# Kernel optimization log

Hardware: AMD Instinct MI355X
Metric: run time of the kernel (lower is better)

The kernel has to match this reference:

```python
import jax, jax.numpy as jnp
import numpy as np

N, E, D, H, G, C = 50000, 800000, 3, 128, 64, 10

def setup_inputs() -> dict:
    key = jax.random.key(0)
    ks = jax.random.split(key, 10)
    s = 0.1  # small init scale
    return {
        "pos": jax.random.normal(ks[0], (N, D), jnp.float32),
        "edge_index": jax.random.randint(ks[1], (2, E), 0, N, dtype=jnp.int64),
        "batch": jnp.sort(jax.random.randint(ks[2], (N,), 0, G, dtype=jnp.int64)),
        "W1": jax.random.normal(ks[3], (D, H), jnp.float32) * s,
        "b1": jnp.zeros((H,), jnp.float32),
        "W2": jax.random.normal(ks[4], (H, H), jnp.float32) * s,
        "b2": jnp.zeros((H,), jnp.float32),
        "W3": jax.random.normal(ks[5], (H, H), jnp.float32) * s,
        "b3": jnp.zeros((H,), jnp.float32),
        "Wl1": jax.random.normal(ks[6], (H, H // 2), jnp.float32) * s,
        "bl1": jnp.zeros((H // 2,), jnp.float32),
        "Wl2": jax.random.normal(ks[7], (H // 2, C), jnp.float32) * s,
        "bl2": jnp.zeros((C,), jnp.float32),
        "num_graphs": G,
    }

def reference(pos, edge_index, batch, W1, b1, W2, b2, W3, b3, Wl1, bl1, Wl2, bl2, num_graphs):
    n = pos.shape[0]
    loop = jnp.arange(n, dtype=edge_index.dtype)
    # GCN: add self-loops, symmetric normalization deg^-1/2 (A+I) deg^-1/2
    src = jnp.concatenate([edge_index[0], loop])
    dst = jnp.concatenate([edge_index[1], loop])
    deg = jax.ops.segment_sum(jnp.ones(src.shape, pos.dtype), dst, num_segments=n)
    dinv = jax.lax.rsqrt(jnp.maximum(deg, 1e-12))  # deg >= 1 due to self-loops
    norm = dinv[src] * dinv[dst]  # [E+N]

    def gcn(x, W, b):
        h = x @ W                               # [N,F] dense transform first (PyG order)
        msg = h[src] * norm[:, None]            # gather + normalize
        return jax.ops.segment_sum(msg, dst, num_segments=n) + b  # scatter-add

    x = jax.nn.relu(gcn(pos, W1, b1))   # dropout = identity (eval mode)
    x = jax.nn.relu(gcn(x, W2, b2))
    x = jax.nn.relu(gcn(x, W3, b3))
    # global_mean_pool over batch ids
    sums = jax.ops.segment_sum(x, batch, num_segments=num_graphs)
    cnt = jax.ops.segment_sum(jnp.ones((n,), x.dtype), batch, num_segments=num_graphs)
    g = sums / jnp.maximum(cnt, 1.0)[:, None]   # [G,H]
    h = jax.nn.relu(g @ Wl1 + bl1)
    return h @ Wl2 + bl2
```

## Files before the change

kernel.cpp:

```cpp
#include <hip/hip_runtime.h>

#define H 128
#define CAP 64
#define LSTRIDE 136
#define PSTR 132
typedef unsigned int uint32;
typedef unsigned short ushort16;
typedef __attribute__((ext_vector_type(8))) short bf16x8;
typedef __attribute__((ext_vector_type(4))) float f32x4;

static __device__ __forceinline__ ushort16 f2bf(float f){
  uint32 u = __float_as_uint(f);
  uint32 r = (u + 0x7fff + ((u >> 16) & 1)) >> 16;
  return (ushort16)r;
}
static __device__ __forceinline__ float bflo(uint32 u){ return __uint_as_float(u << 16); }
static __device__ __forceinline__ float bfhi(uint32 u){ return __uint_as_float(u & 0xffff0000u); }

__global__ __launch_bounds__(256) void k_setup(int* __restrict__ deg, float* __restrict__ gsum,
                                               const int* __restrict__ batch, int n, int G,
                                               int* __restrict__ gb, int SB,
                                               const float* __restrict__ W2, const float* __restrict__ W3,
                                               ushort16* __restrict__ wp2, ushort16* __restrict__ wp3,
                                               float4* __restrict__ y0,
                                               unsigned short* __restrict__ ybA,
                                               unsigned short* __restrict__ ybB,
                                               uint4* __restrict__ csr4){
  int b = blockIdx.x;
  if (b < SB){
    int i = b*256 + threadIdx.x;
    int T = SB*256;
    uint32 ss = (uint32)n | ((uint32)n << 16);
    int NB = (n+1)*8;
    for (int j = i; j < NB; j += T){
      uint4 v; v.x = ss; v.y = ss; v.z = ss; v.w = ss;
      if ((j & 7) == 0){
        int node = j >> 3;
        v.x = (uint32)((node < n)? node : n) | ((uint32)n << 16);
      }
      csr4[j] = v;
    }
    if (i < n) deg[i] = 1;
    if (i < G*H) gsum[i] = 0.f;
    if (i < H){ ybA[(size_t)n*H + i] = 0; ybB[(size_t)n*H + i] = 0; }
    if (i == 0) y0[n] = make_float4(0.f, 0.f, 0.f, 0.f);
    if (i <= G){
      int lo = 0, hi = n;
      while (lo < hi){ int m = (lo + hi) >> 1; if (batch[m] < i) lo = m + 1; else hi = m; }
      gb[i] = lo;
    }
  } else {
    int gid = (b - SB)*256 + threadIdx.x;
    const float* W = (gid < 2048) ? W2 : W3;
    ushort16* wp   = (gid < 2048) ? wp2 : wp3;
    int tid = gid & 2047;
    int frag = tid >> 6, lane = tid & 63;
    int kt = frag >> 3, ct = frag & 7;
    int m = lane & 15, quad = lane >> 4;
    const float* wrow = &W[(kt*32 + quad*8)*H + ct*16 + m];
    ushort16 vals[8];
    #pragma unroll
    for (int j = 0; j < 8; j++) vals[j] = f2bf(wrow[j*H]);
    uint4 o;
    o.x = (uint32)vals[0] | ((uint32)vals[1] << 16);
    o.y = (uint32)vals[2] | ((uint32)vals[3] << 16);
    o.z = (uint32)vals[4] | ((uint32)vals[5] << 16);
    o.w = (uint32)vals[6] | ((uint32)vals[7] << 16);
    *(uint4*)&wp[(size_t)tid*8] = o;
  }
}

__global__ __launch_bounds__(256) void k_fill(const int* __restrict__ src, const int* __restrict__ dst,
                                              int E, int* __restrict__ deg,
                                              unsigned short* __restrict__ csr_src){
  int i = blockIdx.x*256 + threadIdx.x;
  if (i < E){
    int d = dst[i];
    int slot = atomicAdd(&deg[d], 1);
    if (slot < CAP) csr_src[((size_t)d << 6) + slot] = (unsigned short)src[i];
  }
}

__global__ __launch_bounds__(256) void k_pre(const int* __restrict__ deg, const float* __restrict__ pos,
                                             float4* __restrict__ y0, int n){
  int i = blockIdx.x*256 + threadIdx.x;
  if (i < n){
    float dv = rsqrtf((float)deg[i]);
    y0[i] = make_float4(pos[3*i]*dv, pos[3*i+1]*dv, pos[3*i+2]*dv, 0.f);
  }
}

__global__ __launch_bounds__(256) void k_layer1(const float4* __restrict__ y0, const int* __restrict__ deg,
      const unsigned short* __restrict__ csr_src,
      const float* __restrict__ W1, const float* __restrict__ b1,
      ushort16* __restrict__ y1, int n){
  int node = blockIdx.x*256 + threadIdx.x;
  if (node >= n) return;
  int cnt = deg[node];
  int lo = node << 6;
  int hi = lo + ((cnt + 7) & ~7);
  float x=0.f, y=0.f, z=0.f;
  uint4 iv = *(const uint4*)&csr_src[lo];
  for (int e = lo; e < hi; e += 8){
    uint4 ivn = *(const uint4*)&csr_src[e + 8];
    int s0 = iv.x & 0xffff, s1 = iv.x >> 16;
    int s2 = iv.y & 0xffff, s3 = iv.y >> 16;
    int s4 = iv.z & 0xffff, s5 = iv.z >> 16;
    int s6 = iv.w & 0xffff, s7 = iv.w >> 16;
    float4 v0 = y0[s0], v1 = y0[s1], v2 = y0[s2], v3 = y0[s3];
    float4 v4 = y0[s4], v5 = y0[s5], v6 = y0[s6], v7 = y0[s7];
    x += ((v0.x+v1.x)+(v2.x+v3.x)) + ((v4.x+v5.x)+(v6.x+v7.x));
    y += ((v0.y+v1.y)+(v2.y+v3.y)) + ((v4.y+v5.y)+(v6.y+v7.y));
    z += ((v0.z+v1.z)+(v2.z+v3.z)) + ((v4.z+v5.z)+(v6.z+v7.z));
    iv = ivn;
  }
  float dn = rsqrtf((float)cnt);
  x *= dn; y *= dn; z *= dn;
  ushort16* rowp = &y1[(size_t)node*H];
  for (int c8 = 0; c8 < 16; c8++){
    float4 wa0 = *(const float4*)&W1[c8*8];
    float4 wa1 = *(const float4*)&W1[c8*8+4];
    float4 wb0 = *(const float4*)&W1[H + c8*8];
    float4 wb1 = *(const float4*)&W1[H + c8*8+4];
    float4 wc0 = *(const float4*)&W1[2*H + c8*8];
    float4 wc1 = *(const float4*)&W1[2*H + c8*8+4];
    float4 bb0 = *(const float4*)&b1[c8*8];
    float4 bb1 = *(const float4*)&b1[c8*8+4];
    float o0 = fmaxf(x*wa0.x + y*wb0.x + z*wc0.x + bb0.x, 0.f) * dn;
    float o1 = fmaxf(x*wa0.y + y*wb0.y + z*wc0.y + bb0.y, 0.f) * dn;
    float o2 = fmaxf(x*wa0.z + y*wb0.z + z*wc0.z + bb0.z, 0.f) * dn;
    float o3 = fmaxf(x*wa0.w + y*wb0.w + z*wc0.w + bb0.w, 0.f) * dn;
    float o4 = fmaxf(x*wa1.x + y*wb1.x + z*wc1.x + bb1.x, 0.f) * dn;
    float o5 = fmaxf(x*wa1.y + y*wb1.y + z*wc1.y + bb1.y, 0.f) * dn;
    float o6 = fmaxf(x*wa1.z + y*wb1.z + z*wc1.z + bb1.z, 0.f) * dn;
    float o7 = fmaxf(x*wa1.w + y*wb1.w + z*wc1.w + bb1.w, 0.f) * dn;
    uint4 o;
    o.x = (uint32)f2bf(o0) | ((uint32)f2bf(o1) << 16);
    o.y = (uint32)f2bf(o2) | ((uint32)f2bf(o3) << 16);
    o.z = (uint32)f2bf(o4) | ((uint32)f2bf(o5) << 16);
    o.w = (uint32)f2bf(o6) | ((uint32)f2bf(o7) << 16);
    *(uint4*)&rowp[c8*8] = o;
  }
}

template<int POOL>
__global__ __launch_bounds__(256) void k_aggdense(const ushort16* __restrict__ y, const int* __restrict__ deg,
      const unsigned short* __restrict__ csr_src, const ushort16* __restrict__ wp,
      const float* __restrict__ bias,
      ushort16* __restrict__ yout, const int* __restrict__ batch, float* __restrict__ gsum, int n){
  __shared__ unsigned short As[16*LSTRIDE];
  __shared__ float pool[POOL ? 16*PSTR : 1];
  __shared__ unsigned short outs[POOL ? 1 : 16*PSTR];
  __shared__ int sbatch[POOL ? 16 : 1];
  __shared__ float sdinv[POOL ? 1 : 16];
  int tid = threadIdx.x;
  int node16 = blockIdx.x*16;
  int nl = tid >> 4;
  int node = node16 + nl;
  int f8 = (tid & 15) * 8;

  if (tid < 16){
    int nn = node16 + tid;
    if (POOL) sbatch[tid] = (nn < n) ? batch[nn] : -1;
    else      sdinv[tid]  = (nn < n) ? rsqrtf((float)deg[nn]) : 0.f;
  }

  float a0=0,a1=0,a2=0,a3=0,a4=0,a5=0,a6=0,a7=0;
  float dn = 0.f;
  #define ADDU(u) { a0+=bflo(u.x); a1+=bfhi(u.x); a2+=bflo(u.y); a3+=bfhi(u.y); \
                    a4+=bflo(u.z); a5+=bfhi(u.z); a6+=bflo(u.w); a7+=bfhi(u.w); }
  if (node < n){
    int cnt = deg[node];
    int lo = node << 6;
    int hi = lo + ((cnt + 7) & ~7);
    dn = rsqrtf((float)cnt);
    uint4 iv = *(const uint4*)&csr_src[lo];
    for (int e = lo; e < hi; e += 8){
      uint4 ivn = *(const uint4*)&csr_src[e + 8];
      int s0 = iv.x & 0xffff, s1 = iv.x >> 16;
      int s2 = iv.y & 0xffff, s3 = iv.y >> 16;
      int s4 = iv.z & 0xffff, s5 = iv.z >> 16;
      int s6 = iv.w & 0xffff, s7 = iv.w >> 16;
      uint4 u0 = *(const uint4*)&y[(size_t)s0*H + f8];
      uint4 u1 = *(const uint4*)&y[(size_t)s1*H + f8];
      uint4 u2 = *(const uint4*)&y[(size_t)s2*H + f8];
      uint4 u3 = *(const uint4*)&y[(size_t)s3*H + f8];
      uint4 u4 = *(const uint4*)&y[(size_t)s4*H + f8];
      uint4 u5 = *(const uint4*)&y[(size_t)s5*H + f8];
      uint4 u6 = *(const uint4*)&y[(size_t)s6*H + f8];
      uint4 u7 = *(const uint4*)&y[(size_t)s7*H + f8];
      ADDU(u0); ADDU(u1); ADDU(u2); ADDU(u3);
      ADDU(u4); ADDU(u5); ADDU(u6); ADDU(u7);
      iv = ivn;
    }
  }
  #undef ADDU
  uint4 o;
  o.x = (uint32)f2bf(a0*dn) | ((uint32)f2bf(a1*dn) << 16);
  o.y = (uint32)f2bf(a2*dn) | ((uint32)f2bf(a3*dn) << 16);
  o.z = (uint32)f2bf(a4*dn) | ((uint32)f2bf(a5*dn) << 16);
  o.w = (uint32)f2bf(a6*dn) | ((uint32)f2bf(a7*dn) << 16);
  *(uint4*)&As[nl*LSTRIDE + f8] = o;
  __syncthreads();

  int wave = tid >> 6;
  int lane = tid & 63;
  int m = lane & 15, quad = lane >> 4;
  f32x4 acc0 = {0.f,0.f,0.f,0.f}, acc1 = {0.f,0.f,0.f,0.f};
  int ct0 = wave*2, ct1 = wave*2 + 1;
  #pragma unroll
  for (int kt = 0; kt < 4; kt++){
    bf16x8 af = *(const bf16x8*)&As[m*LSTRIDE + kt*32 + quad*8];
    bf16x8 b0 = *(const bf16x8*)&wp[(size_t)((kt*8+ct0)*64 + lane)*8];
    bf16x8 b1 = *(const bf16x8*)&wp[(size_t)((kt*8+ct1)*64 + lane)*8];
    acc0 = __builtin_amdgcn_mfma_f32_16x16x32_bf16(af, b0, acc0, 0, 0, 0);
    acc1 = __builtin_amdgcn_mfma_f32_16x16x32_bf16(af, b1, acc1, 0, 0, 0);
  }
  #pragma unroll
  for (int j = 0; j < 2; j++){
    int ct = wave*2 + j;
    int col = ct*16 + m;
    float bv = bias[col];
    f32x4 ac = j ? acc1 : acc0;
    #pragma unroll
    for (int r = 0; r < 4; r++){
      int rl = quad*4 + r;
      int orow = node16 + rl;
      if (orow < n){
        float v = fmaxf(ac[r] + bv, 0.f);
        if (POOL) pool[rl*PSTR + col] = v;
        else      outs[rl*PSTR + col] = f2bf(v * sdinv[rl]);
      }
    }
  }
  __syncthreads();
  if (POOL){
    int col = tid & 127;
    int half = tid >> 7;
    float run = 0.f; int gprev = -1;
    for (int r = half*8; r < half*8 + 8; r++){
      int g = sbatch[r];
      if (g < 0) break;
      if (g != gprev){
        if (gprev >= 0) atomicAdd(&gsum[gprev*H + col], run);
        run = 0.f; gprev = g;
      }
      run += pool[r*PSTR + col];
    }
    if (gprev >= 0) atomicAdd(&gsum[gprev*H + col], run);
  } else {
    int row = tid >> 4;
    int orow = node16 + row;
    if (orow < n){
      const unsigned short* sp = &outs[row*PSTR + f8];
      uint4 v;
      v.x = (uint32)sp[0] | ((uint32)sp[1] << 16);
      v.y = (uint32)sp[2] | ((uint32)sp[3] << 16);
      v.z = (uint32)sp[4] | ((uint32)sp[5] << 16);
      v.w = (uint32)sp[6] | ((uint32)sp[7] << 16);
      *(uint4*)&yout[(size_t)orow*H + f8] = v;
    }
  }
}

__global__ __launch_bounds__(64) void k_head(const float* __restrict__ gsum, const int* __restrict__ gb,
            const float* __restrict__ Wl1, const float* __restrict__ bl1,
            const float* __restrict__ Wl2, const float* __restrict__ bl2,
            float* __restrict__ out){
  int g = blockIdx.x;
  int t = threadIdx.x;
  __shared__ float gs[H];
  __shared__ float h1[64];
  float inv = 1.f / fmaxf((float)(gb[g+1] - gb[g]), 1.f);
  gs[t]      = gsum[g*H + t]      * inv;
  gs[64 + t] = gsum[g*H + 64 + t] * inv;
  __syncthreads();
  float acc = bl1[t];
  for (int k = 0; k < H; k++) acc += gs[k] * Wl1[k*64 + t];
  h1[t] = fmaxf(acc, 0.f);
  __syncthreads();
  if (t < 10){
    float o = bl2[t];
    for (int j = 0; j < 64; j++) o += h1[j] * Wl2[j*10 + t];
    out[g*10 + t] = o;
  }
}

extern "C" void kernel_launch(void* const* d_in, const int* in_sizes, int n_in,
                              void* d_out, int out_size, void* d_ws, size_t ws_size,
                              hipStream_t stream){
  const float* pos = (const float*)d_in[0];
  const int*  ei   = (const int*)d_in[1];
  const int*  batch= (const int*)d_in[2];
  const float* W1 = (const float*)d_in[3];
  const float* b1 = (const float*)d_in[4];
  const float* W2 = (const float*)d_in[5];
  const float* b2 = (const float*)d_in[6];
  const float* W3 = (const float*)d_in[7];
  const float* b3 = (const float*)d_in[8];
  const float* Wl1 = (const float*)d_in[9];
  const float* bl1 = (const float*)d_in[10];
  const float* Wl2 = (const float*)d_in[11];
  const float* bl2 = (const float*)d_in[12];
  float* out = (float*)d_out;

  int N = in_sizes[0] / 3;
  int E = in_sizes[1] / 2;
  int G = out_size / 10;
  int SB = (N + 255) / 256;

  char* p = (char*)d_ws;
  auto carve = [&](size_t bytes)->char* { char* q = p; p += (bytes + 255) & ~(size_t)255; return q; };
  int*            deg     = (int*)     carve(sizeof(int)    * (size_t)N);
  int*            gb      = (int*)     carve(sizeof(int)    * (size_t)(G+1));
  float*          gsum    = (float*)   carve(sizeof(float)  * (size_t)G * H);
  unsigned short* csr_src = (unsigned short*)carve(sizeof(unsigned short) * (size_t)(N+1) * CAP);
  float4*         y0      = (float4*)  carve(sizeof(float4) * (size_t)(N+1));
  ushort16*       ybufA   = (ushort16*)carve(sizeof(ushort16) * (size_t)(N+1) * H);
  ushort16*       ybufB   = (ushort16*)carve(sizeof(ushort16) * (size_t)(N+1) * H);
  ushort16*       wp2     = (ushort16*)carve(sizeof(ushort16) * 16384);
  ushort16*       wp3     = (ushort16*)carve(sizeof(ushort16) * 16384);

  const int* src = ei;
  const int* dst = ei + E;

  hipLaunchKernelGGL(k_setup, dim3(SB + 16), dim3(256), 0, stream,
                     deg, gsum, batch, N, G, gb, SB, W2, W3, wp2, wp3,
                     y0, (unsigned short*)ybufA, (unsigned short*)ybufB, (uint4*)csr_src);

  hipLaunchKernelGGL(k_fill, dim3((E+255)/256), dim3(256), 0, stream, src, dst, E, deg, csr_src);

  hipLaunchKernelGGL(k_pre, dim3((N+255)/256), dim3(256), 0, stream, deg, pos, y0, N);

  hipLaunchKernelGGL(k_layer1, dim3((N+255)/256), dim3(256), 0, stream, y0, deg, csr_src, W1, b1, ybufA, N);

  hipLaunchKernelGGL(k_aggdense<0>, dim3((N+15)/16), dim3(256), 0, stream,
                     ybufA, deg, csr_src, wp2, b2, ybufB, (const int*)nullptr, (float*)nullptr, N);

  hipLaunchKernelGGL(k_aggdense<1>, dim3((N+15)/16), dim3(256), 0, stream,
                     ybufB, deg, csr_src, wp3, b3, (ushort16*)nullptr, batch, gsum, N);

  hipLaunchKernelGGL(k_head, dim3(G), dim3(64), 0, stream, gsum, gb, Wl1, bl1, Wl2, bl2, out);
}
```

Baseline: 233.6 us.

## Drop CSR padding prefill, handle self-loop and tail explicitly, vectorize fill

Removes the setup pass that pre-filled the whole padded CSR (N*64 entries) with self-loop and sentinel indices. Degree now starts at zero, the self-loop is added explicitly in the aggregation kernels, and the partial last chunk masks unused slots to the zero sentinel row. k_fill also processes four edges per thread using vector loads. The goal is to cut roughly 6.4MB of initialization writes, in exchange for extra branching in the gather kernels; the code also now caps the neighbor count at CAP explicitly.

New measurement: 226.5 us. -3.0%, faster.

```diff
diff --git a/kernel.cpp b/kernel.cpp
--- a/kernel.cpp
+++ b/kernel.cpp
@@ -24,23 +24,11 @@
                                                ushort16* __restrict__ wp2, ushort16* __restrict__ wp3,
                                                float4* __restrict__ y0,
                                                unsigned short* __restrict__ ybA,
-                                               unsigned short* __restrict__ ybB,
-                                               uint4* __restrict__ csr4){
+                                               unsigned short* __restrict__ ybB){
   int b = blockIdx.x;
   if (b < SB){
     int i = b*256 + threadIdx.x;
-    int T = SB*256;
-    uint32 ss = (uint32)n | ((uint32)n << 16);
-    int NB = (n+1)*8;
-    for (int j = i; j < NB; j += T){
-      uint4 v; v.x = ss; v.y = ss; v.z = ss; v.w = ss;
-      if ((j & 7) == 0){
-        int node = j >> 3;
-        v.x = (uint32)((node < n)? node : n) | ((uint32)n << 16);
-      }
-      csr4[j] = v;
-    }
-    if (i < n) deg[i] = 1;
+    if (i < n) deg[i] = 0;
     if (i < G*H) gsum[i] = 0.f;
     if (i < H){ ybA[(size_t)n*H + i] = 0; ybB[(size_t)n*H + i] = 0; }
     if (i == 0) y0[n] = make_float4(0.f, 0.f, 0.f, 0.f);
@@ -73,11 +61,24 @@
 __global__ __launch_bounds__(256) void k_fill(const int* __restrict__ src, const int* __restrict__ dst,
                                               int E, int* __restrict__ deg,
                                               unsigned short* __restrict__ csr_src){
-  int i = blockIdx.x*256 + threadIdx.x;
-  if (i < E){
-    int d = dst[i];
-    int slot = atomicAdd(&deg[d], 1);
-    if (slot < CAP) csr_src[((size_t)d << 6) + slot] = (unsigned short)src[i];
+  int base = (blockIdx.x*256 + threadIdx.x) * 4;
+  if (base + 3 < E){
+    int4 d = *(const int4*)&dst[base];
+    int4 s = *(const int4*)&src[base];
+    int t0 = atomicAdd(&deg[d.x], 1);
+    int t1 = atomicAdd(&deg[d.y], 1);
+    int t2 = atomicAdd(&deg[d.z], 1);
+    int t3 = atomicAdd(&deg[d.w], 1);
+    if (t0 < CAP) csr_src[((size_t)d.x << 6) + t0] = (unsigned short)s.x;
+    if (t1 < CAP) csr_src[((size_t)d.y << 6) + t1] = (unsigned short)s.y;
+    if (t2 < CAP) csr_src[((size_t)d.z << 6) + t2] = (unsigned short)s.z;
+    if (t3 < CAP) csr_src[((size_t)d.w << 6) + t3] = (unsigned short)s.w;
+  } else if (base < E){
+    for (int i = base; i < E; i++){
+      int d = dst[i];
+      int t = atomicAdd(&deg[d], 1);
+      if (t < CAP) csr_src[((size_t)d << 6) + t] = (unsigned short)src[i];
+    }
   }
 }
 
@@ -85,7 +86,7 @@
                                              float4* __restrict__ y0, int n){
   int i = blockIdx.x*256 + threadIdx.x;
   if (i < n){
-    float dv = rsqrtf((float)deg[i]);
+    float dv = rsqrtf((float)(deg[i] + 1));
     y0[i] = make_float4(pos[3*i]*dv, pos[3*i+1]*dv, pos[3*i+2]*dv, 0.f);
   }
 }
@@ -98,23 +99,42 @@
   if (node >= n) return;
   int cnt = deg[node];
   int lo = node << 6;
-  int hi = lo + ((cnt + 7) & ~7);
-  float x=0.f, y=0.f, z=0.f;
-  uint4 iv = *(const uint4*)&csr_src[lo];
-  for (int e = lo; e < hi; e += 8){
-    uint4 ivn = *(const uint4*)&csr_src[e + 8];
-    int s0 = iv.x & 0xffff, s1 = iv.x >> 16;
-    int s2 = iv.y & 0xffff, s3 = iv.y >> 16;
-    int s4 = iv.z & 0xffff, s5 = iv.z >> 16;
-    int s6 = iv.w & 0xffff, s7 = iv.w >> 16;
-    float4 v0 = y0[s0], v1 = y0[s1], v2 = y0[s2], v3 = y0[s3];
-    float4 v4 = y0[s4], v5 = y0[s5], v6 = y0[s6], v7 = y0[s7];
-    x += ((v0.x+v1.x)+(v2.x+v3.x)) + ((v4.x+v5.x)+(v6.x+v7.x));
-    y += ((v0.y+v1.y)+(v2.y+v3.y)) + ((v4.y+v5.y)+(v6.y+v7.y));
-    z += ((v0.z+v1.z)+(v2.z+v3.z)) + ((v4.z+v5.z)+(v6.z+v7.z));
-    iv = ivn;
-  }
-  float dn = rsqrtf((float)cnt);
+  float4 own = y0[node];
+  float x = own.x, y = own.y, z = own.z;
+  int mm = cnt > CAP ? CAP : cnt;
+  int nfull = mm >> 3, rem = mm & 7;
+  #define GADD(s0,s1,s2,s3,s4,s5,s6,s7) { \
+    float4 v0 = y0[s0], v1 = y0[s1], v2 = y0[s2], v3 = y0[s3]; \
+    float4 v4 = y0[s4], v5 = y0[s5], v6 = y0[s6], v7 = y0[s7]; \
+    x += ((v0.x+v1.x)+(v2.x+v3.x)) + ((v4.x+v5.x)+(v6.x+v7.x)); \
+    y += ((v0.y+v1.y)+(v2.y+v3.y)) + ((v4.y+v5.y)+(v6.y+v7.y)); \
+    z += ((v0.z+v1.z)+(v2.z+v3.z)) + ((v4.z+v5.z)+(v6.z+v7.z)); }
+  if (rem){
+    uint4 iv = *(const uint4*)&csr_src[lo + nfull*8];
+    int s0 = (int)(iv.x & 0xffff);
+    int s1 = (1 < rem)? (int)(iv.x >> 16)    : n;
+    int s2 = (2 < rem)? (int)(iv.y & 0xffff) : n;
+    int s3 = (3 < rem)? (int)(iv.y >> 16)    : n;
+    int s4 = (4 < rem)? (int)(iv.z & 0xffff) : n;
+    int s5 = (5 < rem)? (int)(iv.z >> 16)    : n;
+    int s6 = (6 < rem)? (int)(iv.w & 0xffff) : n;
+    int s7 = (7 < rem)? (int)(iv.w >> 16)    : n;
+    GADD(s0,s1,s2,s3,s4,s5,s6,s7);
+  }
+  if (nfull){
+    uint4 iv = *(const uint4*)&csr_src[lo];
+    for (int c = 0; c < nfull; c++){
+      uint4 nx = *(const uint4*)&csr_src[lo + c*8 + 8];
+      int s0 = iv.x & 0xffff, s1 = iv.x >> 16;
+      int s2 = iv.y & 0xffff, s3 = iv.y >> 16;
+      int s4 = iv.z & 0xffff, s5 = iv.z >> 16;
+      int s6 = iv.w & 0xffff, s7 = iv.w >> 16;
+      GADD(s0,s1,s2,s3,s4,s5,s6,s7);
+      iv = nx;
+    }
+  }
+  #undef GADD
+  float dn = rsqrtf((float)(cnt + 1));
   x *= dn; y *= dn; z *= dn;
   ushort16* rowp = &y1[(size_t)node*H];
   for (int c8 = 0; c8 < 16; c8++){
@@ -162,38 +182,58 @@
   if (tid < 16){
     int nn = node16 + tid;
     if (POOL) sbatch[tid] = (nn < n) ? batch[nn] : -1;
-    else      sdinv[tid]  = (nn < n) ? rsqrtf((float)deg[nn]) : 0.f;
+    else      sdinv[tid]  = (nn < n) ? rsqrtf((float)(deg[nn] + 1)) : 0.f;
   }
 
   float a0=0,a1=0,a2=0,a3=0,a4=0,a5=0,a6=0,a7=0;
   float dn = 0.f;
   #define ADDU(u) { a0+=bflo(u.x); a1+=bfhi(u.x); a2+=bflo(u.y); a3+=bfhi(u.y); \
                     a4+=bflo(u.z); a5+=bfhi(u.z); a6+=bflo(u.w); a7+=bfhi(u.w); }
+  #define GATHER8(s0,s1,s2,s3,s4,s5,s6,s7) { \
+    uint4 u0 = *(const uint4*)&y[(size_t)(s0)*H + f8]; \
+    uint4 u1 = *(const uint4*)&y[(size_t)(s1)*H + f8]; \
+    uint4 u2 = *(const uint4*)&y[(size_t)(s2)*H + f8]; \
+    uint4 u3 = *(const uint4*)&y[(size_t)(s3)*H + f8]; \
+    uint4 u4 = *(const uint4*)&y[(size_t)(s4)*H + f8]; \
+    uint4 u5 = *(const uint4*)&y[(size_t)(s5)*H + f8]; \
+    uint4 u6 = *(const uint4*)&y[(size_t)(s6)*H + f8]; \
+    uint4 u7 = *(const uint4*)&y[(size_t)(s7)*H + f8]; \
+    ADDU(u0); ADDU(u1); ADDU(u2); ADDU(u3); \
+    ADDU(u4); ADDU(u5); ADDU(u6); ADDU(u7); }
   if (node < n){
     int cnt = deg[node];
     int lo = node << 6;
-    int hi = lo + ((cnt + 7) & ~7);
-    dn = rsqrtf((float)cnt);
-    uint4 iv = *(const uint4*)&csr_src[lo];
-    for (int e = lo; e < hi; e += 8){
-      uint4 ivn = *(const uint4*)&csr_src[e + 8];
-      int s0 = iv.x & 0xffff, s1 = iv.x >> 16;
-      int s2 = iv.y & 0xffff, s3 = iv.y >> 16;
-      int s4 = iv.z & 0xffff, s5 = iv.z >> 16;
-      int s6 = iv.w & 0xffff, s7 = iv.w >> 16;
-      uint4 u0 = *(const uint4*)&y[(size_t)s0*H + f8];
-      uint4 u1 = *(const uint4*)&y[(size_t)s1*H + f8];
-      uint4 u2 = *(const uint4*)&y[(size_t)s2*H + f8];
-      uint4 u3 = *(const uint4*)&y[(size_t)s3*H + f8];
-      uint4 u4 = *(const uint4*)&y[(size_t)s4*H + f8];
-      uint4 u5 = *(const uint4*)&y[(size_t)s5*H + f8];
-      uint4 u6 = *(const uint4*)&y[(size_t)s6*H + f8];
-      uint4 u7 = *(const uint4*)&y[(size_t)s7*H + f8];
-      ADDU(u0); ADDU(u1); ADDU(u2); ADDU(u3);
-      ADDU(u4); ADDU(u5); ADDU(u6); ADDU(u7);
-      iv = ivn;
-    }
-  }
+    dn = rsqrtf((float)(cnt + 1));
+    uint4 uo = *(const uint4*)&y[(size_t)node*H + f8];
+    ADDU(uo);
+    int mm = cnt > CAP ? CAP : cnt;
+    int nfull = mm >> 3, rem = mm & 7;
+    if (rem){
+      uint4 iv = *(const uint4*)&csr_src[lo + nfull*8];
+      int s0 = (int)(iv.x & 0xffff);
+      int s1 = (1 < rem)? (int)(iv.x >> 16)    : n;
+      int s2 = (2 < rem)? (int)(iv.y & 0xffff) : n;
+      int s3 = (3 < rem)? (int)(iv.y >> 16)    : n;
+      int s4 = (4 < rem)? (int)(iv.z & 0xffff) : n;
+      int s5 = (5 < rem)? (int)(iv.z >> 16)    : n;
+      int s6 = (6 < rem)? (int)(iv.w & 0xffff) : n;
+      int s7 = (7 < rem)? (int)(iv.w >> 16)    : n;
+      GATHER8(s0,s1,s2,s3,s4,s5,s6,s7);
+    }
+    if (nfull){
+      uint4 iv = *(const uint4*)&csr_src[lo];
+      for (int c = 0; c < nfull; c++){
+        uint4 nx = *(const uint4*)&csr_src[lo + c*8 + 8];
+        int s0 = iv.x & 0xffff, s1 = iv.x >> 16;
+        int s2 = iv.y & 0xffff, s3 = iv.y >> 16;
+        int s4 = iv.z & 0xffff, s5 = iv.z >> 16;
+        int s6 = iv.w & 0xffff, s7 = iv.w >> 16;
+        GATHER8(s0,s1,s2,s3,s4,s5,s6,s7);
+        iv = nx;
+      }
+    }
+  }
+  #undef GATHER8
   #undef ADDU
   uint4 o;
   o.x = (uint32)f2bf(a0*dn) | ((uint32)f2bf(a1*dn) << 16);
@@ -326,9 +366,9 @@
 
   hipLaunchKernelGGL(k_setup, dim3(SB + 16), dim3(256), 0, stream,
                      deg, gsum, batch, N, G, gb, SB, W2, W3, wp2, wp3,
-                     y0, (unsigned short*)ybufA, (unsigned short*)ybufB, (uint4*)csr_src);
-
-  hipLaunchKernelGGL(k_fill, dim3((E+255)/256), dim3(256), 0, stream, src, dst, E, deg, csr_src);
+                     y0, (unsigned short*)ybufA, (unsigned short*)ybufB);
+
+  hipLaunchKernelGGL(k_fill, dim3(((E+3)/4 + 255)/256), dim3(256), 0, stream, src, dst, E, deg, csr_src);
 
   hipLaunchKernelGGL(k_pre, dim3((N+255)/256), dim3(256), 0, stream, deg, pos, y0, N);
 
```
